# Kernel tuning notes

Hardware: AMD Instinct MI355X
Metric: run time of the kernel (lower is better)

Reference implementation:

```python
import jax, jax.numpy as jnp
import numpy as np

DIM = 1024
NUM_STAGES = 10  # log2(DIM)
N_TOKENS = 16384


def setup_inputs() -> dict:
    key = jax.random.key(0)
    k1, k2 = jax.random.split(key)
    x = jax.random.normal(k1, (N_TOKENS, DIM), dtype=jnp.float32)
    angles = jax.random.normal(k2, (NUM_STAGES, DIM // 2), dtype=jnp.float32)
    return {"x": x, "angles": angles}


def reference(x, angles):
    dim = x.shape[-1]
    num_stages = angles.shape[0]
    orig_shape = x.shape
    y = x.reshape(-1, dim)
    for stage in range(num_stages):  # fixed log2(dim) stages
        span = 2 ** (stage + 1)
        half = span // 2
        y = y.reshape(-1, dim // span, span)
        left, right = y[..., :half], y[..., half:]
        theta = angles[stage].reshape(1, dim // span, half)
        cos_t, sin_t = jnp.cos(theta), jnp.sin(theta)
        y = jnp.concatenate(
            [cos_t * left + sin_t * right, -sin_t * left + cos_t * right], axis=-1
        ).reshape(-1, dim)
    return y.reshape(orig_shape)
```

## Files before the change

### kernel.cpp

```cpp
#include <hip/hip_runtime.h>
#include <math.h>

#define DIM     1024
#define NSTAGES 10
#define HALFD   512
#define TABN    (NSTAGES * HALFD)

__global__ void bf_prep(const float* __restrict__ ang, float* __restrict__ ws) {
    int i = blockIdx.x * blockDim.x + threadIdx.x;
    if (i < TABN) {
        float s, c;
        sincosf(ang[i], &s, &c);
        ws[i]        = c;
        ws[TABN + i] = s;
    }
}

__device__ __forceinline__ float xor1(float f) {
    return __builtin_bit_cast(float,
        __builtin_amdgcn_update_dpp(0, __builtin_bit_cast(int, f), 0xB1, 0xF, 0xF, true));
}
__device__ __forceinline__ float xor2(float f) {
    return __builtin_bit_cast(float,
        __builtin_amdgcn_update_dpp(0, __builtin_bit_cast(int, f), 0x4E, 0xF, 0xF, true));
}
__device__ __forceinline__ float xor4(float f) {
    return __builtin_bit_cast(float,
        __builtin_amdgcn_ds_swizzle(__builtin_bit_cast(int, f), 0x101F));
}
__device__ __forceinline__ float xor8(float f) {
    return __builtin_bit_cast(float,
        __builtin_amdgcn_ds_swizzle(__builtin_bit_cast(int, f), 0x201F));
}

__device__ __forceinline__ void pl16(float& a, float& b) {
    asm("v_permlane16_swap_b32 %0, %1" : "+v"(a), "+v"(b));
}
__device__ __forceinline__ void pl32(float& a, float& b) {
    asm("v_permlane32_swap_b32 %0, %1" : "+v"(a), "+v"(b));
}

#define XSTAGE(S, XORF)                                                    \
    {                                                                      \
        constexpr int m = 1 << ((S) - 2);                                  \
        const float* cT = cosT + (S) * HALFD;                              \
        const float* sT = sinT + (S) * HALFD;                              \
        const int l0 = lane & ~m;                                          \
        const float sgn = (lane & m) ? -1.0f : 1.0f;                       \
        _Pragma("unroll")                                                  \
        for (int c = 0; c < 4; ++c) {                                      \
            const int p0 = (((c << (7 - (S))) + (l0 >> ((S) - 1))) << (S)) \
                         + 4 * (l0 & (m - 1));                             \
            float4 C = *(const float4*)&cT[p0];                            \
            float4 Sv = *(const float4*)&sT[p0];                           \
            Sv.x *= sgn; Sv.y *= sgn; Sv.z *= sgn; Sv.w *= sgn;            \
            _Pragma("unroll")                                              \
            for (int r = 0; r < 2; ++r) {                                  \
                float4 u = v[r][c];                                        \
                float tx = XORF(u.x), ty = XORF(u.y);                      \
                float tz = XORF(u.z), tw = XORF(u.w);                      \
                v[r][c].x = C.x * u.x + Sv.x * tx;                         \
                v[r][c].y = C.y * u.y + Sv.y * ty;                         \
                v[r][c].z = C.z * u.z + Sv.z * tz;                         \
                v[r][c].w = C.w * u.w + Sv.w * tw;                         \
            }                                                              \
        }                                                                  \
    }

#define PLPAIR(A, B, Cv, Svv, PLFN)                                        \
    {                                                                      \
        float a_ = (A), b_ = (B);                                          \
        PLFN(a_, b_);                                                      \
        float an_ = Cv * a_ + Svv * b_;                        \
        float bn_ = Cv * b_ - Svv * a_;                        \
        PLFN(an_, bn_);                                                    \
        (A) = an_; (B) = bn_;                                              \
    }

#define XSTAGE_PL(S, PLFN, SELBIT)                                         \
    {                                                                      \
        constexpr int m = 1 << ((S) - 2);                                  \
        const float* cT = cosT + (S) * HALFD;                              \
        const float* sT = sinT + (S) * HALFD;                              \
        const int l0 = lane & ~m;                                          \
        const bool hi = (lane & (SELBIT)) != 0;                            \
        _Pragma("unroll")                                                  \
        for (int c = 0; c < 4; ++c) {                                      \
            const int p0 = (((c << (7 - (S))) + (l0 >> ((S) - 1))) << (S)) \
                         + 4 * (l0 & (m - 1));                             \
            float4 C = *(const float4*)&cT[p0];                            \
            float4 Sv = *(const float4*)&sT[p0];                           \
            float cxy = hi ? C.y : C.x,  sxy = hi ? Sv.y : Sv.x;           \
            float czw = hi ? C.w : C.z,  szw = hi ? Sv.w : Sv.z;           \
            _Pragma("unroll")                                              \
            for (int r = 0; r < 2; ++r) {                                  \
                PLPAIR(v[r][c].x, v[r][c].y, cxy, sxy, PLFN)               \
                PLPAIR(v[r][c].z, v[r][c].w, czw, szw, PLFN)               \
            }                                                              \
        }                                                                  \
    }

__device__ __forceinline__ void processBatch(float4 (&v)[2][4],
                                             const float* __restrict__ cosT,
                                             const float* __restrict__ sinT,
                                             int lane)
{
    #pragma unroll
    for (int s01 = 0; s01 < 2; ++s01) {
        const float* cT = cosT + s01 * HALFD;
        const float* sT = sinT + s01 * HALFD;
        #pragma unroll
        for (int c = 0; c < 4; ++c) {
            const int p = 128 * c + 2 * lane;
            float2 cc = *(const float2*)&cT[p];
            float2 ss = *(const float2*)&sT[p];
            #pragma unroll
            for (int r = 0; r < 2; ++r) {
                float4 u = v[r][c];
                if (s01 == 0) {
                    v[r][c].x = cc.x * u.x + ss.x * u.y;
                    v[r][c].y = cc.x * u.y - ss.x * u.x;
                    v[r][c].z = cc.y * u.z + ss.y * u.w;
                    v[r][c].w = cc.y * u.w - ss.y * u.z;
                } else {
                    v[r][c].x = cc.x * u.x + ss.x * u.z;
                    v[r][c].z = cc.x * u.z - ss.x * u.x;
                    v[r][c].y = cc.y * u.y + ss.y * u.w;
                    v[r][c].w = cc.y * u.w - ss.y * u.y;
                }
            }
        }
    }

    XSTAGE(2, xor1)
    XSTAGE(3, xor2)
    XSTAGE(4, xor4)
    XSTAGE(5, xor8)
    XSTAGE_PL(6, pl16, 16)
    XSTAGE_PL(7, pl32, 32)

    {
        const float* cT = cosT + 8 * HALFD;
        const float* sT = sinT + 8 * HALFD;
        #pragma unroll
        for (int g = 0; g < 2; ++g) {
            const int p0 = 256 * g + 4 * lane;
            float4 C = *(const float4*)&cT[p0];
            float4 S = *(const float4*)&sT[p0];
            #pragma unroll
            for (int r = 0; r < 2; ++r) {
                float4 L = v[r][2 * g], Rr = v[r][2 * g + 1];
                v[r][2 * g].x     = C.x * L.x + S.x * Rr.x;
                v[r][2 * g].y     = C.y * L.y + S.y * Rr.y;
                v[r][2 * g].z     = C.z * L.z + S.z * Rr.z;
                v[r][2 * g].w     = C.w * L.w + S.w * Rr.w;
                v[r][2 * g + 1].x = C.x * Rr.x - S.x * L.x;
                v[r][2 * g + 1].y = C.y * Rr.y - S.y * L.y;
                v[r][2 * g + 1].z = C.z * Rr.z - S.z * L.z;
                v[r][2 * g + 1].w = C.w * Rr.w - S.w * L.w;
            }
        }
    }

    {
        const float* cT = cosT + 9 * HALFD;
        const float* sT = sinT + 9 * HALFD;
        #pragma unroll
        for (int g = 0; g < 2; ++g) {
            const int p0 = 256 * g + 4 * lane;
            float4 C = *(const float4*)&cT[p0];
            float4 S = *(const float4*)&sT[p0];
            #pragma unroll
            for (int r = 0; r < 2; ++r) {
                float4 L = v[r][g], Rr = v[r][g + 2];
                v[r][g].x     = C.x * L.x + S.x * Rr.x;
                v[r][g].y     = C.y * L.y + S.y * Rr.y;
                v[r][g].z     = C.z * L.z + S.z * Rr.z;
                v[r][g].w     = C.w * L.w + S.w * Rr.w;
                v[r][g + 2].x = C.x * Rr.x - S.x * L.x;
                v[r][g + 2].y = C.y * Rr.y - S.y * L.y;
                v[r][g + 2].z = C.z * Rr.z - S.z * L.z;
                v[r][g + 2].w = C.w * Rr.w - S.w * L.w;
            }
        }
    }
}

__global__ __launch_bounds__(256) void bf_main(
    const float* __restrict__ x,
    const float* __restrict__ tab,
    float* __restrict__ out)
{
    __shared__ __align__(16) float cosT[TABN];
    __shared__ __align__(16) float sinT[TABN];
    const int tid  = threadIdx.x;
    const int lane = tid & 63;
    const int gwid = blockIdx.x * 4 + (tid >> 6);

    {
        const float4* s4 = (const float4*)tab;
        float4* c4 = (float4*)cosT;
        float4* n4 = (float4*)sinT;
        #pragma unroll
        for (int i = 0; i < TABN / 4 / 256; ++i) {
            const int idx = i * 256 + tid;
            c4[idx] = s4[idx];
            n4[idx] = s4[TABN / 4 + idx];
        }
    }

    const float4* xp = (const float4*)x   + (size_t)gwid * 4 * (DIM / 4) + lane;
    float4*       op = (float4*)      out + (size_t)gwid * 4 * (DIM / 4) + lane;

    float4 v0[2][4];
    #pragma unroll
    for (int r = 0; r < 2; ++r)
        #pragma unroll
        for (int c = 0; c < 4; ++c)
            v0[r][c] = xp[r * 256 + c * 64];

    __syncthreads();

    {
        float4 (&v)[2][4] = v0;
        processBatch(v, cosT, sinT, lane);
    }
    #pragma unroll
    for (int r = 0; r < 2; ++r)
        #pragma unroll
        for (int c = 0; c < 4; ++c)
            op[r * 256 + c * 64] = v0[r][c];

    asm volatile("" ::: "memory");

    float4 v1[2][4];
    #pragma unroll
    for (int r = 0; r < 2; ++r)
        #pragma unroll
        for (int c = 0; c < 4; ++c)
            v1[r][c] = xp[(2 + r) * 256 + c * 64];

    {
        float4 (&v)[2][4] = v1;
        processBatch(v, cosT, sinT, lane);
    }
    #pragma unroll
    for (int r = 0; r < 2; ++r)
        #pragma unroll
        for (int c = 0; c < 4; ++c)
            op[(2 + r) * 256 + c * 64] = v1[r][c];
}

extern "C" void kernel_launch(void* const* d_in, const int* in_sizes, int n_in,
                              void* d_out, int out_size, void* d_ws, size_t ws_size,
                              hipStream_t stream) {
    const float* x   = (const float*)d_in[0];
    const float* ang = (const float*)d_in[1];
    float* out = (float*)d_out;

    const int nrows = out_size / DIM;
    const int nblocks = nrows / 16;

    float* tab = (float*)d_ws;
    bf_prep<<<(TABN + 255) / 256, 256, 0, stream>>>(ang, tab);
    bf_main<<<nblocks, 256, 0, stream>>>(x, tab, out);
}
```

Measured before the change: 31.87 us.

## Shrink LDS twiddle table to 8 stages, read stages 0-1 from global

Stages 0 and 1 now read their cos/sin twiddles straight from the global table, so the LDS copy holds only stages 2-9. This cuts shared memory per block from 40KB to 32KB, and launch bounds request 5 blocks per CU to raise occupancy. The xor8 exchange moves from ds_swizzle to a DPP row-mirror variant, and compiler memory fences are placed between stage groups to shape scheduling. The trade-off is extra global or L2 reads for the first two stages and possible register pressure from the occupancy hint.

```diff
diff --git a/kernel.cpp b/kernel.cpp
--- a/kernel.cpp
+++ b/kernel.cpp
@@ -5,6 +5,9 @@
 #define NSTAGES 10
 #define HALFD   512
 #define TABN    (NSTAGES * HALFD)
+#define LTABN   (8 * HALFD)
+
+#define STAGE_FENCE asm volatile("" ::: "memory");
 
 __global__ void bf_prep(const float* __restrict__ ang, float* __restrict__ ws) {
     int i = blockIdx.x * blockDim.x + threadIdx.x;
@@ -30,7 +33,7 @@
 }
 __device__ __forceinline__ float xor8(float f) {
     return __builtin_bit_cast(float,
-        __builtin_amdgcn_ds_swizzle(__builtin_bit_cast(int, f), 0x201F));
+        __builtin_amdgcn_update_dpp(0, __builtin_bit_cast(int, f), 0x128, 0xF, 0xF, true));
 }
 
 __device__ __forceinline__ void pl16(float& a, float& b) {
@@ -43,8 +46,8 @@
 #define XSTAGE(S, XORF)                                                    \
     {                                                                      \
         constexpr int m = 1 << ((S) - 2);                                  \
-        const float* cT = cosT + (S) * HALFD;                              \
-        const float* sT = sinT + (S) * HALFD;                              \
+        const float* cT = cosT + ((S) - 2) * HALFD;                        \
+        const float* sT = sinT + ((S) - 2) * HALFD;                        \
         const int l0 = lane & ~m;                                          \
         const float sgn = (lane & m) ? -1.0f : 1.0f;                       \
         _Pragma("unroll")                                                  \
@@ -80,8 +83,8 @@
 #define XSTAGE_PL(S, PLFN, SELBIT)                                         \
     {                                                                      \
         constexpr int m = 1 << ((S) - 2);                                  \
-        const float* cT = cosT + (S) * HALFD;                              \
-        const float* sT = sinT + (S) * HALFD;                              \
+        const float* cT = cosT + ((S) - 2) * HALFD;                        \
+        const float* sT = sinT + ((S) - 2) * HALFD;                        \
         const int l0 = lane & ~m;                                          \
         const bool hi = (lane & (SELBIT)) != 0;                            \
         _Pragma("unroll")                                                  \
@@ -101,19 +104,20 @@
     }
 
 __device__ __forceinline__ void processBatch(float4 (&v)[2][4],
+                                             const float* __restrict__ tab,
                                              const float* __restrict__ cosT,
                                              const float* __restrict__ sinT,
                                              int lane)
 {
     #pragma unroll
     for (int s01 = 0; s01 < 2; ++s01) {
-        const float* cT = cosT + s01 * HALFD;
-        const float* sT = sinT + s01 * HALFD;
+        const float* cG = tab + s01 * HALFD;
+        const float* sG = tab + TABN + s01 * HALFD;
         #pragma unroll
         for (int c = 0; c < 4; ++c) {
             const int p = 128 * c + 2 * lane;
-            float2 cc = *(const float2*)&cT[p];
-            float2 ss = *(const float2*)&sT[p];
+            float2 cc = *(const float2*)&cG[p];
+            float2 ss = *(const float2*)&sG[p];
             #pragma unroll
             for (int r = 0; r < 2; ++r) {
                 float4 u = v[r][c];
@@ -131,17 +135,20 @@
             }
         }
     }
+    STAGE_FENCE
 
     XSTAGE(2, xor1)
     XSTAGE(3, xor2)
     XSTAGE(4, xor4)
+    STAGE_FENCE
     XSTAGE(5, xor8)
     XSTAGE_PL(6, pl16, 16)
     XSTAGE_PL(7, pl32, 32)
-
-    {
-        const float* cT = cosT + 8 * HALFD;
-        const float* sT = sinT + 8 * HALFD;
+    STAGE_FENCE
+
+    {
+        const float* cT = cosT + 6 * HALFD;
+        const float* sT = sinT + 6 * HALFD;
         #pragma unroll
         for (int g = 0; g < 2; ++g) {
             const int p0 = 256 * g + 4 * lane;
@@ -163,8 +170,8 @@
     }
 
     {
-        const float* cT = cosT + 9 * HALFD;
-        const float* sT = sinT + 9 * HALFD;
+        const float* cT = cosT + 7 * HALFD;
+        const float* sT = sinT + 7 * HALFD;
         #pragma unroll
         for (int g = 0; g < 2; ++g) {
             const int p0 = 256 * g + 4 * lane;
@@ -186,13 +193,13 @@
     }
 }
 
-__global__ __launch_bounds__(256) void bf_main(
+__global__ __launch_bounds__(256, 5) void bf_main(
     const float* __restrict__ x,
     const float* __restrict__ tab,
     float* __restrict__ out)
 {
-    __shared__ __align__(16) float cosT[TABN];
-    __shared__ __align__(16) float sinT[TABN];
+    __shared__ __align__(16) float cosT[LTABN];
+    __shared__ __align__(16) float sinT[LTABN];
     const int tid  = threadIdx.x;
     const int lane = tid & 63;
     const int gwid = blockIdx.x * 4 + (tid >> 6);
@@ -201,11 +208,11 @@
         const float4* s4 = (const float4*)tab;
         float4* c4 = (float4*)cosT;
         float4* n4 = (float4*)sinT;
-        #pragma unroll
-        for (int i = 0; i < TABN / 4 / 256; ++i) {
+        #pragma unroll 1
+        for (int i = 0; i < LTABN / 4 / 256; ++i) {
             const int idx = i * 256 + tid;
-            c4[idx] = s4[idx];
-            n4[idx] = s4[TABN / 4 + idx];
+            c4[idx] = s4[idx + 2 * HALFD / 4];
+            n4[idx] = s4[idx + (TABN + 2 * HALFD) / 4];
         }
     }
 
@@ -223,7 +230,7 @@
 
     {
         float4 (&v)[2][4] = v0;
-        processBatch(v, cosT, sinT, lane);
+        processBatch(v, tab, cosT, sinT, lane);
     }
     #pragma unroll
     for (int r = 0; r < 2; ++r)
@@ -242,7 +249,7 @@
 
     {
         float4 (&v)[2][4] = v1;
-        processBatch(v, cosT, sinT, lane);
+        processBatch(v, tab, cosT, sinT, lane);
     }
     #pragma unroll
     for (int r = 0; r < 2; ++r)
```

After: 36.99 us. 16.1% more time.
